# Kernel tuning notes

Measured on AMD Instinct MI355X. Metric: run time of the kernel, lower is better.

## Reference

```python
import jax, jax.numpy as jnp
import numpy as np

N, P, D_IN, K, D_H = 4, 20000, 1024, 8, 64


def setup_inputs() -> dict:
    key = jax.random.key(0)
    ks = jax.random.split(key, 10)
    inp = {
        "x": jax.random.normal(ks[0], (N, P, D_IN), dtype=jnp.float32),
        "centroids": jax.random.normal(ks[1], (K, D_IN), dtype=jnp.float32),
        # proj_pre: Linear(in_dim, 64) + ReLU  (W stored as [in, out])
        "W_pre": jax.random.normal(ks[2], (D_IN, D_H), dtype=jnp.float32) / np.sqrt(D_IN),
        "b_pre": jnp.zeros((D_H,), dtype=jnp.float32),
        # attention: Linear(64,32) -> Tanh -> Linear(32,1)
        "W_a1": jax.random.normal(ks[3], (D_H, 32), dtype=jnp.float32) / np.sqrt(D_H),
        "b_a1": jnp.zeros((32,), dtype=jnp.float32),
        "W_a2": jax.random.normal(ks[4], (32, 1), dtype=jnp.float32) / np.sqrt(32.0),
        "b_a2": jnp.zeros((1,), dtype=jnp.float32),
        # proj_out: Linear(64,32) + ReLU (+ Dropout, identity at eval)
        "W_out": jax.random.normal(ks[5], (D_H, 32), dtype=jnp.float32) / np.sqrt(D_H),
        "b_out": jnp.zeros((32,), dtype=jnp.float32),
    }
    return inp


def reference(x, centroids, W_pre, b_pre, W_a1, b_a1, W_a2, b_a2, W_out, b_out):
    # --- cdist-based hard cluster assignment ---------------------------------
    # ||x - c||: use the expanded form to avoid an [n,p,K,d] broadcast.
    x2 = jnp.sum(x * x, axis=-1)                       # [n, p]
    c2 = jnp.sum(centroids * centroids, axis=-1)       # [K]
    d2 = x2[..., None] + c2 - 2.0 * jnp.einsum('npd,kd->npk', x, centroids)
    dist = jnp.sqrt(jnp.maximum(d2, 0.0))              # [n, p, K]

    wc = jax.nn.softmax(1e7 / dist, axis=-1)           # softmax(1e7/dist)
    wc = (wc > 0.5).astype(x.dtype)                    # hard assignment
    # F.normalize(p=1, dim=1): divide by per-(n,K) patch count (eps=1e-12)
    wc = wc / jnp.maximum(jnp.sum(wc, axis=1, keepdims=True), 1e-12)
    mask = jnp.sum(wc, axis=1) == 0                    # [n, K] empty clusters

    # --- per-patch projection -------------------------------------------------
    xp = jax.nn.relu(x @ W_pre + b_pre)                # [n, p, 64]

    # --- cluster pooling + attention ------------------------------------------
    x_cls = jnp.einsum('npd,nph->nhd', xp, wc)         # [n, K, 64]
    A = (jnp.tanh(x_cls @ W_a1 + b_a1) @ W_a2 + b_a2)[..., 0]  # [n, K]
    A = jnp.where(mask, jnp.asarray(-100000.0, A.dtype), A)
    wa = jax.nn.softmax(A, axis=-1)                    # [n, K]
    pooled = jnp.einsum('nhd,nh->nd', x_cls, wa)       # [n, 64]

    enc_cls = jax.nn.relu(pooled @ W_out + b_out)      # [n, 32] (dropout = eval)
    enc_seq = xp.reshape(-1, xp.shape[-1])             # [(n*p), 64]
    return enc_cls, enc_seq, enc_seq
```

## Files before the change

### kernel.cpp

```cpp
#include <hip/hip_runtime.h>
#include <math.h>

#define N_  4
#define P_  20000
#define DIN 1024
#define K_  8
#define DH  64
#define BP  128
#define NT  5

typedef float  f32x4 __attribute__((ext_vector_type(4)));
typedef short  s16x8 __attribute__((ext_vector_type(8)));
typedef unsigned int u32x4 __attribute__((ext_vector_type(4)));
typedef unsigned short ushort_t;


union FragU { u32x4 u; s16x8 s; };

__device__ __forceinline__ void async_ld16(const float* g, float* l) {
  __builtin_amdgcn_global_load_lds(
      (const __attribute__((address_space(1))) unsigned int*)g,
      (__attribute__((address_space(3))) unsigned int*)l, 16, 0, 0);
}

__global__ __launch_bounds__(512) void k_pre(const float* __restrict__ W_pre,
                                             const float* __restrict__ centroids,
                                             float* __restrict__ ws) {
  const int t = threadIdx.x;
  const int b = blockIdx.x;
  if (b < 80) {
    const int c = b;
    ushort_t* Bth = (ushort_t*)(ws + 4096);
    ushort_t* Btl = (ushort_t*)(ws + 45056);
    for (int d = t; d < DIN; d += 512) {
      float v = 0.f;
      if (c < 64)      v = W_pre[(size_t)d * DH + c];
      else if (c < 72) v = centroids[(size_t)(c - 64) * DIN + d];
      unsigned u = __float_as_uint(v);
      unsigned r = u + 0x7FFFu + ((u >> 16) & 1u);
      unsigned hb = r & 0xFFFF0000u;
      float lo = v - __uint_as_float(hb);
      unsigned ul = __float_as_uint(lo);
      unsigned rl = ul + 0x7FFFu + ((ul >> 16) & 1u);
      Bth[(size_t)c * DIN + d] = (ushort_t)(hb >> 16);
      Btl[(size_t)c * DIN + d] = (ushort_t)(rl >> 16);
    }
  } else {
    int* gcnt = (int*)(ws + 2048);
    for (int i = t; i < N_ * K_ * DH; i += 512) ws[i] = 0.f;
    if (t < N_ * K_) gcnt[t] = 0;
    const int w = t >> 6, lane = t & 63;
    float s = 0.f;
    for (int d = lane; d < DIN; d += 64) {
      float v = centroids[(size_t)w * DIN + d];
      s += v * v;
    }
    for (int off = 32; off > 0; off >>= 1) s += __shfl_down(s, off, 64);
    if (lane == 0) ws[2080 + w] = s;
  }
}

__global__ __launch_bounds__(256) void k_main(
    const float* __restrict__ x, const float* __restrict__ b_pre,
    float* __restrict__ out1, float* __restrict__ out2, float* __restrict__ ws) {
  __shared__ float smem[2 * BP * 64];
  __shared__ float sc[BP * 9];
  __shared__ int   assign_s[BP];
  __shared__ int   cnt8[K_];
  __shared__ float c2s[K_];

  const int t = threadIdx.x;
  const int w = t >> 6, l = t & 63;
  const int m = l & 15, q4 = l >> 4;
  const int quad8 = q4 << 3;
  const int n = blockIdx.y;
  const int p0 = blockIdx.x * BP;
  const int validP = (P_ - p0) < BP ? (P_ - p0) : BP;

  const ushort_t* Bth = (const ushort_t*)(ws + 4096);
  const ushort_t* Btl = (const ushort_t*)(ws + 45056);

  if (t < K_) { cnt8[t] = 0; c2s[t] = ws[2080 + t]; }

  f32x4 acc[2][NT];
#pragma unroll
  for (int rg = 0; rg < 2; ++rg)
#pragma unroll
    for (int tl = 0; tl < NT; ++tl) acc[rg][tl] = (f32x4){0.f, 0.f, 0.f, 0.f};

  const float* xbase = x + (size_t)n * P_ * DIN;

  const float* gsrc[8];
  float* ldst[8];
#pragma unroll
  for (int ii = 0; ii < 8; ++ii) {
    const int R = w * 32 + ii * 4;
    const int row = R + q4;
    const int g = m ^ (row & 15);
    int gp = p0 + row; gp = gp < P_ ? gp : P_ - 1;
    gsrc[ii] = xbase + (size_t)gp * DIN + 4 * g;
    ldst[ii] = smem + R * 64;
  }

#pragma unroll
  for (int ii = 0; ii < 8; ++ii) async_ld16(gsrc[ii], ldst[ii]);

  for (int ch = 0; ch < 16; ++ch) {
    __syncthreads();
    if (ch < 15) {
      const int nb = (ch + 1) & 1;
#pragma unroll
      for (int ii = 0; ii < 8; ++ii)
        async_ld16(gsrc[ii] + (ch + 1) * 64, ldst[ii] + nb * 8192);
    }
    const float* bufp = smem + (ch & 1) * 8192;

#pragma unroll
    for (int kk = 0; kk < 2; ++kk) {
      const int kb = ch * 64 + kk * 32 + quad8;
      FragU bh[NT], bl[NT];
#pragma unroll
      for (int tl = 0; tl < NT; ++tl) {
        const size_t off = (size_t)(tl * 16 + m) * DIN + kb;
        bh[tl].u = *(const u32x4*)(Bth + off);
        bl[tl].u = *(const u32x4*)(Btl + off);
      }
#pragma unroll
      for (int rg = 0; rg < 2; ++rg) {
        const int row = 32 * w + 16 * rg + m;
        const int ga = kk * 8 + (q4 << 1);
        f32x4 a0 = *(const f32x4*)(bufp + row * 64 + 4 * (ga ^ m));
        f32x4 a1 = *(const f32x4*)(bufp + row * 64 + 4 * ((ga + 1) ^ m));
        float f[8];
#pragma unroll
        for (int e = 0; e < 4; ++e) { f[e] = a0[e]; f[4 + e] = a1[e]; }
        FragU ah, al;
#pragma unroll
        for (int q = 0; q < 4; ++q) {
          const unsigned u0 = __float_as_uint(f[2 * q]);
          const unsigned u1 = __float_as_uint(f[2 * q + 1]);
          ah.u[q] = (u0 >> 16) | (u1 & 0xFFFF0000u);
          const float l0 = f[2 * q]     - __uint_as_float(u0 & 0xFFFF0000u);
          const float l1 = f[2 * q + 1] - __uint_as_float(u1 & 0xFFFF0000u);
          al.u[q] = (__float_as_uint(l0) >> 16) | (__float_as_uint(l1) & 0xFFFF0000u);
        }
#pragma unroll
        for (int tl = 0; tl < NT; ++tl) {
          acc[rg][tl] = __builtin_amdgcn_mfma_f32_16x16x32_bf16(ah.s, bh[tl].s, acc[rg][tl], 0, 0, 0);
          acc[rg][tl] = __builtin_amdgcn_mfma_f32_16x16x32_bf16(ah.s, bl[tl].s, acc[rg][tl], 0, 0, 0);
          acc[rg][tl] = __builtin_amdgcn_mfma_f32_16x16x32_bf16(al.s, bh[tl].s, acc[rg][tl], 0, 0, 0);
        }
      }
    }
  }
  __syncthreads();

#pragma unroll
  for (int tl = 0; tl < 4; ++tl) {
    const int col = tl * 16 + m;
    const float bb = b_pre[col];
#pragma unroll
    for (int rg = 0; rg < 2; ++rg) {
#pragma unroll
      for (int r = 0; r < 4; ++r) {
        const int row = 32 * w + 16 * rg + (q4 << 2) + r;
        float v = acc[rg][tl][r] + bb;
        v = v > 0.f ? v : 0.f;
        smem[row * 65 + col] = v;
        if (row < validP) {
          const size_t o = (((size_t)(n * P_ + p0 + row)) << 6) + col;
          out1[o] = v;
          out2[o] = v;
        }
      }
    }
  }
  if (m < K_) {
#pragma unroll
    for (int rg = 0; rg < 2; ++rg)
#pragma unroll
      for (int r = 0; r < 4; ++r) {
        const int row = 32 * w + 16 * rg + (q4 << 2) + r;
        sc[row * 9 + m] = c2s[m] - 2.f * acc[rg][4][r];
      }
  }
  __syncthreads();

  if (t < BP) {
    int a = -1;
    if (t < validP) {
      float best = 3.4e38f; int bk = 0;
#pragma unroll
      for (int k = 0; k < K_; ++k) {
        const float v = sc[t * 9 + k];
        if (v < best) { best = v; bk = k; }
      }
      a = bk;
      atomicAdd(&cnt8[bk], 1);
    }
    assign_s[t] = a;
  }
  __syncthreads();

  for (int task = t; task < K_ * DH; task += 256) {
    const int k = task >> 6, j = task & 63;
    float s = 0.f;
    for (int p = 0; p < BP; ++p)
      s += (assign_s[p] == k) ? smem[p * 65 + j] : 0.f;
    if (s != 0.f) atomicAdd(&ws[(n * K_ + k) * DH + j], s);
  }
  if (t < K_ && cnt8[t] > 0) atomicAdd((int*)(ws + 2048) + n * K_ + t, cnt8[t]);
}

__global__ __launch_bounds__(256) void k_final(
    const float* __restrict__ W_a1, const float* __restrict__ b_a1,
    const float* __restrict__ W_a2, const float* __restrict__ b_a2,
    const float* __restrict__ W_out, const float* __restrict__ b_out,
    const float* __restrict__ ws, float* __restrict__ enc_cls) {
  __shared__ float xc[N_ * K_ * DH];
  __shared__ float wa[N_ * K_];
  __shared__ float As[N_ * K_];
  __shared__ int   cnts[N_ * K_];
  __shared__ float pooled[N_ * DH];
  const int t = threadIdx.x;
  const float* gsum = ws;
  const int* gcnt = (const int*)(ws + 2048);

  if (t < N_ * K_) cnts[t] = gcnt[t];
  __syncthreads();
  for (int i = t; i < N_ * K_ * DH; i += 256) {
    const int nk = i >> 6;
    const int c = cnts[nk];
    xc[i] = (c > 0) ? gsum[i] / (float)c : 0.f;
  }
  __syncthreads();
  if (t < N_ * K_) {
    float a = b_a2[0];
    for (int h = 0; h < 32; ++h) {
      float z = b_a1[h];
      for (int j = 0; j < DH; ++j) z += xc[t * DH + j] * W_a1[j * 32 + h];
      a += tanhf(z) * W_a2[h];
    }
    As[t] = (cnts[t] > 0) ? a : -100000.f;
  }
  __syncthreads();
  if (t < N_) {
    float mx = -3.4e38f;
    for (int k = 0; k < K_; ++k) mx = fmaxf(mx, As[t * K_ + k]);
    float ssum = 0.f;
    float e[K_];
    for (int k = 0; k < K_; ++k) { e[k] = expf(As[t * K_ + k] - mx); ssum += e[k]; }
    for (int k = 0; k < K_; ++k) wa[t * K_ + k] = e[k] / ssum;
  }
  __syncthreads();
  {
    const int n = t >> 6, j = t & 63;
    float s = 0.f;
    for (int k = 0; k < K_; ++k) s += xc[(n * K_ + k) * DH + j] * wa[n * K_ + k];
    pooled[t] = s;
  }
  __syncthreads();
  if (t < N_ * 32) {
    const int n = t >> 5, o = t & 31;
    float s = b_out[o];
    for (int j = 0; j < DH; ++j) s += pooled[n * DH + j] * W_out[j * 32 + o];
    enc_cls[n * 32 + o] = fmaxf(s, 0.f);
  }
}

extern "C" void kernel_launch(void* const* d_in, const int* in_sizes, int n_in,
                              void* d_out, int out_size, void* d_ws, size_t ws_size,
                              hipStream_t stream) {
  const float* x         = (const float*)d_in[0];
  const float* centroids = (const float*)d_in[1];
  const float* W_pre     = (const float*)d_in[2];
  const float* b_pre     = (const float*)d_in[3];
  const float* W_a1      = (const float*)d_in[4];
  const float* b_a1      = (const float*)d_in[5];
  const float* W_a2      = (const float*)d_in[6];
  const float* b_a2      = (const float*)d_in[7];
  const float* W_out     = (const float*)d_in[8];
  const float* b_out     = (const float*)d_in[9];

  float* out     = (float*)d_out;
  float* ws      = (float*)d_ws;
  float* enc_cls = out;
  float* out1    = out + N_ * 32;
  float* out2    = out + N_ * 32 + (size_t)N_ * P_ * DH;

  hipLaunchKernelGGL(k_pre, dim3(81), dim3(512), 0, stream, W_pre, centroids, ws);
  hipLaunchKernelGGL(k_main, dim3((P_ + BP - 1) / BP, N_), dim3(256), 0, stream,
                     x, b_pre, out1, out2, ws);
  hipLaunchKernelGGL(k_final, dim3(1), dim3(256), 0, stream,
                     W_a1, b_a1, W_a2, b_a2, W_out, b_out, ws, enc_cls);
}
```

Baseline: 591.2 us.

## Load x fragments directly from global instead of LDS double buffering

```diff
diff --git a/kernel.cpp b/kernel.cpp
--- a/kernel.cpp
+++ b/kernel.cpp
@@ -16,12 +16,6 @@
 
 
 union FragU { u32x4 u; s16x8 s; };
-
-__device__ __forceinline__ void async_ld16(const float* g, float* l) {
-  __builtin_amdgcn_global_load_lds(
-      (const __attribute__((address_space(1))) unsigned int*)g,
-      (__attribute__((address_space(3))) unsigned int*)l, 16, 0, 0);
-}
 
 __global__ __launch_bounds__(512) void k_pre(const float* __restrict__ W_pre,
                                              const float* __restrict__ centroids,
@@ -60,19 +54,33 @@
   }
 }
 
-__global__ __launch_bounds__(256) void k_main(
+__device__ __forceinline__ void cvt_split(const f32x4 a0, const f32x4 a1,
+                                          FragU& ah, FragU& al) {
+  float f[8];
+#pragma unroll
+  for (int e = 0; e < 4; ++e) { f[e] = a0[e]; f[4 + e] = a1[e]; }
+#pragma unroll
+  for (int q = 0; q < 4; ++q) {
+    const unsigned u0 = __float_as_uint(f[2 * q]);
+    const unsigned u1 = __float_as_uint(f[2 * q + 1]);
+    ah.u[q] = (u0 >> 16) | (u1 & 0xFFFF0000u);
+    const float l0 = f[2 * q]     - __uint_as_float(u0 & 0xFFFF0000u);
+    const float l1 = f[2 * q + 1] - __uint_as_float(u1 & 0xFFFF0000u);
+    al.u[q] = (__float_as_uint(l0) >> 16) | (__float_as_uint(l1) & 0xFFFF0000u);
+  }
+}
+
+__global__ __launch_bounds__(256, 3) void k_main(
     const float* __restrict__ x, const float* __restrict__ b_pre,
     float* __restrict__ out1, float* __restrict__ out2, float* __restrict__ ws) {
-  __shared__ float smem[2 * BP * 64];
+  __shared__ float xp[BP * 65];
   __shared__ float sc[BP * 9];
   __shared__ int   assign_s[BP];
   __shared__ int   cnt8[K_];
-  __shared__ float c2s[K_];
 
   const int t = threadIdx.x;
   const int w = t >> 6, l = t & 63;
   const int m = l & 15, q4 = l >> 4;
-  const int quad8 = q4 << 3;
   const int n = blockIdx.y;
   const int p0 = blockIdx.x * BP;
   const int validP = (P_ - p0) < BP ? (P_ - p0) : BP;
@@ -80,7 +88,7 @@
   const ushort_t* Bth = (const ushort_t*)(ws + 4096);
   const ushort_t* Btl = (const ushort_t*)(ws + 45056);
 
-  if (t < K_) { cnt8[t] = 0; c2s[t] = ws[2080 + t]; }
+  if (t < K_) cnt8[t] = 0;
 
   f32x4 acc[2][NT];
 #pragma unroll
@@ -88,72 +96,55 @@
 #pragma unroll
     for (int tl = 0; tl < NT; ++tl) acc[rg][tl] = (f32x4){0.f, 0.f, 0.f, 0.f};
 
-  const float* xbase = x + (size_t)n * P_ * DIN;
-
-  const float* gsrc[8];
-  float* ldst[8];
-#pragma unroll
-  for (int ii = 0; ii < 8; ++ii) {
-    const int R = w * 32 + ii * 4;
-    const int row = R + q4;
-    const int g = m ^ (row & 15);
-    int gp = p0 + row; gp = gp < P_ ? gp : P_ - 1;
-    gsrc[ii] = xbase + (size_t)gp * DIN + 4 * g;
-    ldst[ii] = smem + R * 64;
-  }
-
-#pragma unroll
-  for (int ii = 0; ii < 8; ++ii) async_ld16(gsrc[ii], ldst[ii]);
-
-  for (int ch = 0; ch < 16; ++ch) {
-    __syncthreads();
-    if (ch < 15) {
-      const int nb = (ch + 1) & 1;
-#pragma unroll
-      for (int ii = 0; ii < 8; ++ii)
-        async_ld16(gsrc[ii] + (ch + 1) * 64, ldst[ii] + nb * 8192);
-    }
-    const float* bufp = smem + (ch & 1) * 8192;
-
-#pragma unroll
-    for (int kk = 0; kk < 2; ++kk) {
-      const int kb = ch * 64 + kk * 32 + quad8;
-      FragU bh[NT], bl[NT];
-#pragma unroll
-      for (int tl = 0; tl < NT; ++tl) {
-        const size_t off = (size_t)(tl * 16 + m) * DIN + kb;
-        bh[tl].u = *(const u32x4*)(Bth + off);
-        bl[tl].u = *(const u32x4*)(Btl + off);
-      }
-#pragma unroll
-      for (int rg = 0; rg < 2; ++rg) {
-        const int row = 32 * w + 16 * rg + m;
-        const int ga = kk * 8 + (q4 << 1);
-        f32x4 a0 = *(const f32x4*)(bufp + row * 64 + 4 * (ga ^ m));
-        f32x4 a1 = *(const f32x4*)(bufp + row * 64 + 4 * ((ga + 1) ^ m));
-        float f[8];
-#pragma unroll
-        for (int e = 0; e < 4; ++e) { f[e] = a0[e]; f[4 + e] = a1[e]; }
-        FragU ah, al;
-#pragma unroll
-        for (int q = 0; q < 4; ++q) {
-          const unsigned u0 = __float_as_uint(f[2 * q]);
-          const unsigned u1 = __float_as_uint(f[2 * q + 1]);
-          ah.u[q] = (u0 >> 16) | (u1 & 0xFFFF0000u);
-          const float l0 = f[2 * q]     - __uint_as_float(u0 & 0xFFFF0000u);
-          const float l1 = f[2 * q + 1] - __uint_as_float(u1 & 0xFFFF0000u);
-          al.u[q] = (__float_as_uint(l0) >> 16) | (__float_as_uint(l1) & 0xFFFF0000u);
-        }
-#pragma unroll
-        for (int tl = 0; tl < NT; ++tl) {
-          acc[rg][tl] = __builtin_amdgcn_mfma_f32_16x16x32_bf16(ah.s, bh[tl].s, acc[rg][tl], 0, 0, 0);
-          acc[rg][tl] = __builtin_amdgcn_mfma_f32_16x16x32_bf16(ah.s, bl[tl].s, acc[rg][tl], 0, 0, 0);
-          acc[rg][tl] = __builtin_amdgcn_mfma_f32_16x16x32_bf16(al.s, bh[tl].s, acc[rg][tl], 0, 0, 0);
-        }
-      }
-    }
-  }
-  __syncthreads();
+  const int r0 = p0 + 32 * w + m;
+  const int r1 = r0 + 16;
+  const int g0 = r0 < P_ ? r0 : P_ - 1;
+  const int g1 = r1 < P_ ? r1 : P_ - 1;
+  const float* xbase = x + (size_t)n * P_ * DIN + q4 * 8;
+  const float* ap0 = xbase + (size_t)g0 * DIN;
+  const float* ap1 = xbase + (size_t)g1 * DIN;
+
+  const ushort_t* bhp[NT];
+  const ushort_t* blp[NT];
+#pragma unroll
+  for (int tl = 0; tl < NT; ++tl) {
+    const size_t off = (size_t)(tl * 16 + m) * DIN + q4 * 8;
+    bhp[tl] = Bth + off;
+    blp[tl] = Btl + off;
+  }
+
+#pragma unroll 4
+  for (int ks = 0; ks < 32; ++ks) {
+    const int ko = ks * 32;
+    const f32x4 a00 = *(const f32x4*)(ap0 + ko);
+    const f32x4 a01 = *(const f32x4*)(ap0 + ko + 4);
+    const f32x4 a10 = *(const f32x4*)(ap1 + ko);
+    const f32x4 a11 = *(const f32x4*)(ap1 + ko + 4);
+    FragU bh[NT], bl[NT];
+#pragma unroll
+    for (int tl = 0; tl < NT; ++tl) {
+      bh[tl].u = *(const u32x4*)(bhp[tl] + ko);
+      bl[tl].u = *(const u32x4*)(blp[tl] + ko);
+    }
+    FragU ah0, al0, ah1, al1;
+    cvt_split(a00, a01, ah0, al0);
+    cvt_split(a10, a11, ah1, al1);
+#pragma unroll
+    for (int tl = 0; tl < NT; ++tl) {
+      acc[0][tl] = __builtin_amdgcn_mfma_f32_16x16x32_bf16(ah0.s, bh[tl].s, acc[0][tl], 0, 0, 0);
+      acc[1][tl] = __builtin_amdgcn_mfma_f32_16x16x32_bf16(ah1.s, bh[tl].s, acc[1][tl], 0, 0, 0);
+    }
+#pragma unroll
+    for (int tl = 0; tl < NT; ++tl) {
+      acc[0][tl] = __builtin_amdgcn_mfma_f32_16x16x32_bf16(ah0.s, bl[tl].s, acc[0][tl], 0, 0, 0);
+      acc[1][tl] = __builtin_amdgcn_mfma_f32_16x16x32_bf16(ah1.s, bl[tl].s, acc[1][tl], 0, 0, 0);
+    }
+#pragma unroll
+    for (int tl = 0; tl < NT; ++tl) {
+      acc[0][tl] = __builtin_amdgcn_mfma_f32_16x16x32_bf16(al0.s, bh[tl].s, acc[0][tl], 0, 0, 0);
+      acc[1][tl] = __builtin_amdgcn_mfma_f32_16x16x32_bf16(al1.s, bh[tl].s, acc[1][tl], 0, 0, 0);
+    }
+  }
 
 #pragma unroll
   for (int tl = 0; tl < 4; ++tl) {
@@ -166,7 +157,7 @@
         const int row = 32 * w + 16 * rg + (q4 << 2) + r;
         float v = acc[rg][tl][r] + bb;
         v = v > 0.f ? v : 0.f;
-        smem[row * 65 + col] = v;
+        xp[row * 65 + col] = v;
         if (row < validP) {
           const size_t o = (((size_t)(n * P_ + p0 + row)) << 6) + col;
           out1[o] = v;
@@ -176,12 +167,13 @@
     }
   }
   if (m < K_) {
+    const float cc = ws[2080 + m];
 #pragma unroll
     for (int rg = 0; rg < 2; ++rg)
 #pragma unroll
       for (int r = 0; r < 4; ++r) {
         const int row = 32 * w + 16 * rg + (q4 << 2) + r;
-        sc[row * 9 + m] = c2s[m] - 2.f * acc[rg][4][r];
+        sc[row * 9 + m] = cc - 2.f * acc[rg][4][r];
       }
   }
   __syncthreads();
@@ -206,7 +198,7 @@
     const int k = task >> 6, j = task & 63;
     float s = 0.f;
     for (int p = 0; p < BP; ++p)
-      s += (assign_s[p] == k) ? smem[p * 65 + j] : 0.f;
+      s += (assign_s[p] == k) ? xp[p * 65 + j] : 0.f;
     if (s != 0.f) atomicAdd(&ws[(n * K_ + k) * DH + j], s);
   }
   if (t < K_ && cnt8[t] > 0) atomicAdd((int*)(ws + 2048) + n * K_ + t, cnt8[t]);
@@ -218,6 +210,7 @@
     const float* __restrict__ W_out, const float* __restrict__ b_out,
     const float* __restrict__ ws, float* __restrict__ enc_cls) {
   __shared__ float xc[N_ * K_ * DH];
+  __shared__ float zs[N_ * K_ * 32];
   __shared__ float wa[N_ * K_];
   __shared__ float As[N_ * K_];
   __shared__ int   cnts[N_ * K_];
@@ -234,13 +227,16 @@
     xc[i] = (c > 0) ? gsum[i] / (float)c : 0.f;
   }
   __syncthreads();
+  for (int i = t; i < N_ * K_ * 32; i += 256) {
+    const int nk = i >> 5, h = i & 31;
+    float z = b_a1[h];
+    for (int j = 0; j < DH; ++j) z += xc[nk * DH + j] * W_a1[j * 32 + h];
+    zs[i] = tanhf(z) * W_a2[h];
+  }
+  __syncthreads();
   if (t < N_ * K_) {
     float a = b_a2[0];
-    for (int h = 0; h < 32; ++h) {
-      float z = b_a1[h];
-      for (int j = 0; j < DH; ++j) z += xc[t * DH + j] * W_a1[j * 32 + h];
-      a += tanhf(z) * W_a2[h];
-    }
+    for (int h = 0; h < 32; ++h) a += zs[t * 32 + h];
     As[t] = (cnts[t] > 0) ? a : -100000.f;
   }
   __syncthreads();
```

New measurement: 554.3 us. -6.2%, faster.
